# Kernel tuning notes

Hardware: AMD Instinct MI355X
Metric: run time of the kernel (lower is better)

The kernel has to match this reference:

```python
import jax, jax.numpy as jnp
import numpy as np

ALPHA = 0.2  # LeakyReLU negative slope
NEG_INF = -1e30


def _gat_layer(h, adj_mask, W, a, concat):
    # h: [N, Fin], W: [Fin, Fout], a: [2*Fout]
    Wh = h @ W                      # [N, Fout]
    F = W.shape[1]
    # e_ij = LeakyReLU(a[:F] . Wh_i + a[F:] . Wh_j)  -- equivalent to the
    # concat([Wh_i, Wh_j]) @ a formulation, without the N*N*2F tensor.
    src = Wh @ a[:F]                # [N]
    dst = Wh @ a[F:]                # [N]
    e = src[:, None] + dst[None, :]  # [N, N]
    e = jnp.where(e > 0, e, ALPHA * e)  # LeakyReLU
    e = jnp.where(adj_mask, e, NEG_INF)
    att = jax.nn.softmax(e, axis=1)  # [N, N]; dropout inactive (eval mode)
    h_prime = att @ Wh               # [N, Fout]
    return jax.nn.elu(h_prime) if concat else h_prime


def setup_inputs() -> dict:
    key = jax.random.key(0)
    ks = jax.random.split(key, 6)
    N, nfeat, nhid, nheads, nout = 4096, 512, 256, 4, 256
    x = jax.random.normal(ks[0], (N, nfeat), dtype=jnp.float32)
    adj = jax.random.randint(ks[1], (N, N), 0, 2, dtype=jnp.int32)
    W1 = jax.random.normal(ks[2], (nheads, nfeat, nhid), dtype=jnp.float32) * 0.05
    a1 = jax.random.normal(ks[3], (nheads, 2 * nhid), dtype=jnp.float32) * 0.05
    W2 = jax.random.normal(ks[4], (nhid * nheads, nout), dtype=jnp.float32) * 0.05
    a2 = jax.random.normal(ks[5], (2 * nout,), dtype=jnp.float32) * 0.05
    return {"x": x, "adj": adj, "W1": W1, "a1": a1, "W2": W2, "a2": a2}


def reference(x, adj, W1, a1, W2, a2):
    adj_mask = adj != 0  # [N, N] bool
    # Multi-head first layer (concat=True, ELU), vmapped over heads.
    heads = jax.vmap(lambda W, a: _gat_layer(x, adj_mask, W, a, True))(W1, a1)
    # heads: [nheads, N, nhid] -> concat along features: [N, nheads*nhid]
    h = jnp.transpose(heads, (1, 0, 2)).reshape(x.shape[0], -1)
    # Output attention layer (concat=False).
    return _gat_layer(h, adj_mask, W2, a2, False)
```

## Files before the change

kernel.cpp:

```cpp
#include <hip/hip_runtime.h>
#include <hip/hip_bf16.h>
#include <stdint.h>

#define ALPHA 0.2f
#define LOG2E 1.4426950408889634f

typedef __attribute__((ext_vector_type(4))) float f32x4;
typedef __attribute__((ext_vector_type(8))) __bf16 bf16x8;
typedef __attribute__((ext_vector_type(8))) unsigned short u16x8;
typedef __attribute__((ext_vector_type(4))) unsigned short u16x4;
typedef __attribute__((ext_vector_type(4))) unsigned int u32x4;

static __device__ __forceinline__ unsigned short f2bf(float f) {
  unsigned u = __builtin_bit_cast(unsigned, f);
  u += 0x7FFFu + ((u >> 16) & 1u);
  return (unsigned short)(u >> 16);
}
static __device__ __forceinline__ float bf2f(unsigned short h) {
  unsigned u = ((unsigned)h) << 16;
  return __builtin_bit_cast(float, u);
}
static __device__ __forceinline__ float exp2_hw(float x) {
  float r; asm("v_exp_f32 %0, %1" : "=v"(r) : "v"(x)); return r;
}
static __device__ __forceinline__ unsigned int cvt_pk_bf16(float lo, float hi) {
  unsigned int r; asm("v_cvt_pk_bf16_f32 %0, %1, %2" : "=v"(r) : "v"(lo), "v"(hi)); return r;
}
static __device__ __forceinline__ void gl_lds16(const void* g, void* lds) {
  __builtin_amdgcn_global_load_lds(
      (const __attribute__((address_space(1))) unsigned int*)g,
      (__attribute__((address_space(3))) unsigned int*)lds, 16, 0, 0);
}

#define PREP_PACK_END 16384
#define PREP_CAST_END 17408
#define PREP_T1_END   17920
#define PREP_T2_END   18176
#define PREP_WA1_END  18688
#define PREP_GRID     18944

__global__ void k_prep(const int* __restrict__ adj, unsigned int* __restrict__ bits,
                       const float* __restrict__ x, unsigned short* __restrict__ xb,
                       const float* __restrict__ W1, unsigned short* __restrict__ w1t,
                       const float* __restrict__ W2, unsigned short* __restrict__ w2t,
                       const float* __restrict__ a1, float* __restrict__ wa1,
                       const float* __restrict__ a2, float* __restrict__ wa2) {
  __shared__ float tsh[32][33];
  const int b = blockIdx.x, tid = threadIdx.x;
  if (b < PREP_PACK_END) {
    int row = b >> 2, qo = b & 3;
    const int4* ap = (const int4*)(adj + (size_t)row * 4096 + qo * 1024);
    int4 v = ap[tid];
    unsigned n = (unsigned)(v.x != 0) | ((unsigned)(v.y != 0) << 1) |
                 ((unsigned)(v.z != 0) << 2) | ((unsigned)(v.w != 0) << 3);
    unsigned char* nib = (unsigned char*)tsh;
    nib[tid] = (unsigned char)n;
    __syncthreads();
    if (tid < 32) {
      unsigned w = 0;
#pragma unroll
      for (int s = 0; s < 8; ++s) w |= ((unsigned)nib[tid * 8 + s]) << (4 * s);
      bits[(size_t)row * 128 + qo * 32 + tid] = w;
    }
  } else if (b < PREP_CAST_END) {
    int t = (b - PREP_PACK_END) * 256 + tid;
    const f32x4* p = (const f32x4*)(x + (long)t * 8);
    f32x4 va = p[0], vb = p[1];
    u16x8 o;
#pragma unroll
    for (int k = 0; k < 4; ++k) { o[k] = f2bf(va[k]); o[k + 4] = f2bf(vb[k]); }
    *(u16x8*)(xb + (long)t * 8) = o;
  } else if (b < PREP_T2_END) {
    const float* in; unsigned short* out; int K, N, bx, by, bz;
    if (b < PREP_T1_END) {
      int idx = b - PREP_CAST_END;
      bx = idx & 15; by = (idx >> 4) & 7; bz = idx >> 7;
      in = W1; out = w1t; K = 512; N = 256;
    } else {
      int idx = b - PREP_T1_END;
      bx = idx & 31; by = (idx >> 5) & 7; bz = 0;
      in = W2; out = w2t; K = 1024; N = 256;
    }
    long bs = (long)K * N;
    const float* inb = in + bz * bs;
    unsigned short* outb = out + bz * bs;
    int k0 = bx * 32, n0 = by * 32;
    int tx = tid & 31, ty = tid >> 5;
#pragma unroll
    for (int it = 0; it < 4; ++it)
      tsh[ty + it * 8][tx] = inb[(long)(k0 + ty + it * 8) * N + n0 + tx];
    __syncthreads();
#pragma unroll
    for (int it = 0; it < 4; ++it)
      outb[(long)(n0 + ty + it * 8) * K + k0 + tx] = f2bf(tsh[tx][ty + it * 8]);
  } else {
    const float* W; const float* a; float* wa; int headK;
    int bl;
    if (b < PREP_WA1_END) { bl = b - PREP_T2_END; W = W1; a = a1; wa = wa1; headK = 512; }
    else                  { bl = b - PREP_WA1_END; W = W2; a = a2; wa = wa2; headK = 1024; }
    const int F = 256;
    int w = (bl * 256 + tid) >> 6;
    int lane = tid & 63;
    int h = w / headK, fl = w % headK;
    const float* row = W + (size_t)w * F;
    const float* ah = a + (size_t)h * 2 * F;
    float s0 = 0.f, s1 = 0.f;
    for (int fo = lane; fo < F; fo += 64) {
      float wv = row[fo];
      s0 += wv * ah[fo];
      s1 += wv * ah[F + fo];
    }
#pragma unroll
    for (int off = 32; off; off >>= 1) {
      s0 += __shfl_xor(s0, off);
      s1 += __shfl_xor(s1, off);
    }
    if (lane == 0) {
      wa[(size_t)(h * 2 + 0) * headK + fl] = s0;
      wa[(size_t)(h * 2 + 1) * headK + fl] = s1;
    }
  }
}

static __device__ __forceinline__ void gemm_wh_body(
    const unsigned short* __restrict__ A, const unsigned short* __restrict__ BT,
    unsigned short* __restrict__ whT, int K, int i0, int fbase, char* lds) {
  unsigned short* As = (unsigned short*)lds;
  unsigned short* Bs = (unsigned short*)(lds + 8192);
  const int tid = threadIdx.x, lane = tid & 63, wid = tid >> 6;
  const int q = lane >> 4, l15 = lane & 15;
  const int wm = wid >> 1, wn = wid & 1;
  f32x4 acc[2][4] = {};
  const unsigned short* aRow = A + (long)(i0 + (tid >> 2)) * K + (tid & 3) * 8;
  const int cid1 = 256 + tid;
  const unsigned short* bRow0 = BT + (long)(fbase + (tid >> 2)) * K + (tid & 3) * 8;
  const unsigned short* bRow1 = BT + (long)(fbase + (cid1 >> 2)) * K + (cid1 & 3) * 8;

#define GSTAGE(PAR, KK)                                                        \
  gl_lds16(aRow + (KK), lds + (PAR) * 4096 + tid * 16);                        \
  gl_lds16(bRow0 + (KK), lds + 8192 + (PAR) * 8192 + tid * 16);                \
  gl_lds16(bRow1 + (KK), lds + 8192 + (PAR) * 8192 + cid1 * 16);

  GSTAGE(0, 0)
  asm volatile("s_waitcnt vmcnt(0)" ::: "memory");
  __builtin_amdgcn_sched_barrier(0);
  __builtin_amdgcn_s_barrier();
  for (int kk = 0; kk < K; kk += 32) {
    const int par = (kk >> 5) & 1;
    if (kk + 32 < K) { GSTAGE(par ^ 1, kk + 32) }
    bf16x8 af[2], bfr[4];
#pragma unroll
    for (int mi = 0; mi < 2; ++mi)
      af[mi] = *(const bf16x8*)&As[par * 2048 + (wm * 32 + mi * 16 + l15) * 32 + q * 8];
#pragma unroll
    for (int ni = 0; ni < 4; ++ni)
      bfr[ni] = *(const bf16x8*)&Bs[par * 4096 + (wn * 64 + ni * 16 + l15) * 32 + q * 8];
    __builtin_amdgcn_s_setprio(1);
#pragma unroll
    for (int mi = 0; mi < 2; ++mi)
#pragma unroll
      for (int ni = 0; ni < 4; ++ni)
        acc[mi][ni] = __builtin_amdgcn_mfma_f32_16x16x32_bf16(af[mi], bfr[ni], acc[mi][ni], 0, 0, 0);
    __builtin_amdgcn_s_setprio(0);
    asm volatile("s_waitcnt vmcnt(0)" ::: "memory");
    asm volatile("s_waitcnt lgkmcnt(0)" ::: "memory");
    __builtin_amdgcn_sched_barrier(0);
    __builtin_amdgcn_s_barrier();
    __builtin_amdgcn_sched_barrier(0);
  }
#undef GSTAGE
#pragma unroll
  for (int mi = 0; mi < 2; ++mi)
#pragma unroll
    for (int ni = 0; ni < 4; ++ni) {
      int ig = i0 + wm * 32 + mi * 16 + q * 4;
      int fg = fbase + wn * 64 + ni * 16 + l15;
      u16x4 v;
#pragma unroll
      for (int r = 0; r < 4; ++r) v[r] = f2bf(acc[mi][ni][r]);
      *(u16x4*)&whT[(long)fg * 4096 + ig] = v;
    }
}

__global__ void __launch_bounds__(256, 4)
k_l1(const unsigned short* __restrict__ xb, const unsigned short* __restrict__ w1t,
     unsigned short* __restrict__ whT1, const float* __restrict__ wa,
     float* __restrict__ srcv, float* __restrict__ dstv, float* __restrict__ dstva) {
  __shared__ char lds[24576];
  const int b = blockIdx.x, tid = threadIdx.x;
  if (b < 512) {
    int i0 = (b & 63) * 64;
    int fbase = (b >> 7) * 256 + ((b >> 6) & 1) * 128;
    gemm_wh_body(xb, w1t, whT1, 512, i0, fbase, lds);
    return;
  }
  const int mb = b - 512;
  int lane = tid & 63, wid = tid >> 6;
  float wv[8][8];
#pragma unroll
  for (int v = 0; v < 8; ++v)
#pragma unroll
    for (int j = 0; j < 8; ++j) wv[v][j] = wa[v * 512 + lane * 8 + j];
  int base = (mb * 4 + wid) * 4;
  for (int rr = 0; rr < 4; ++rr) {
    int i = base + rr;
    u16x8 xv = *(const u16x8*)(xb + (size_t)i * 512 + lane * 8);
    float xf[8];
#pragma unroll
    for (int j = 0; j < 8; ++j) xf[j] = bf2f(xv[j]);
    float s[8] = {};
#pragma unroll
    for (int v = 0; v < 8; ++v)
#pragma unroll
      for (int j = 0; j < 8; ++j) s[v] += xf[j] * wv[v][j];
#pragma unroll
    for (int v = 0; v < 8; ++v)
#pragma unroll
      for (int off = 32; off; off >>= 1) s[v] += __shfl_xor(s[v], off);
    if (lane == 0) {
#pragma unroll
      for (int h = 0; h < 4; ++h) {
        srcv[h * 4096 + i] = s[h * 2] * LOG2E;
        float d = s[h * 2 + 1] * LOG2E;
        dstv[h * 4096 + i] = d;
        dstva[h * 4096 + i] = ALPHA * d;
      }
    }
  }
}

__global__ void __launch_bounds__(256, 4)
k_l2(const unsigned short* __restrict__ h1, const unsigned short* __restrict__ w2t,
     unsigned short* __restrict__ whT2, const float* __restrict__ wa,
     float* __restrict__ srcv, float* __restrict__ dstv, float* __restrict__ dstva) {
  __shared__ char lds[24576];
  const int b = blockIdx.x;
  if (b < 128) {
    int i0 = (b & 63) * 64;
    int fbase = ((b >> 6) & 1) * 128;
    gemm_wh_body(h1, w2t, whT2, 1024, i0, fbase, lds);
    return;
  }
  const int mb = b - 128;
  int lane = threadIdx.x & 63, wid = threadIdx.x >> 6;
  float wv[2][16];
#pragma unroll
  for (int v = 0; v < 2; ++v)
#pragma unroll
    for (int j = 0; j < 16; ++j) wv[v][j] = wa[v * 1024 + lane * 16 + j];
  int base = (mb * 4 + wid) * 4;
  for (int rr = 0; rr < 4; ++rr) {
    int i = base + rr;
    u16x8 x0 = *(const u16x8*)(h1 + (size_t)i * 1024 + lane * 16);
    u16x8 x1 = *(const u16x8*)(h1 + (size_t)i * 1024 + lane * 16 + 8);
    float s0 = 0.f, s1 = 0.f;
#pragma unroll
    for (int j = 0; j < 8; ++j) {
      float a0 = bf2f(x0[j]), a1 = bf2f(x1[j]);
      s0 += a0 * wv[0][j] + a1 * wv[0][j + 8];
      s1 += a0 * wv[1][j] + a1 * wv[1][j + 8];
    }
#pragma unroll
    for (int off = 32; off; off >>= 1) {
      s0 += __shfl_xor(s0, off);
      s1 += __shfl_xor(s1, off);
    }
    if (lane == 0) {
      srcv[i] = s0 * LOG2E;
      float d = s1 * LOG2E;
      dstv[i] = d;
      dstva[i] = ALPHA * d;
    }
  }
}


#define STAGE(PAR)                                                             \
  _Pragma("unroll")                                                            \
  for (int it = 0; it < 8; ++it)                                               \
    gl_lds16(wh_head + sidx + it * 131072u,                                    \
             (char*)&Bs[PAR][0] + (it * 256 + tid) * 16);                      \
  sidx += 64;

#define PREFETCH(DZ, DA, WB)                                                   \
  _Pragma("unroll")                                                            \
  for (int c4 = 0; c4 < 4; ++c4) {                                             \
    DZ[c4] = *(const f32x4*)(dzp + c4 * 4);                                    \
    DA[c4] = *(const f32x4*)(dap + c4 * 4);                                    \
  }                                                                            \
  WB = *browp;                                                                 \
  dzp += 64; dap += 64; browp += 2;

#define PCOMP(WB, DZ, DA)                                                      \
  {                                                                            \
    unsigned wbv = (WB >> shift) & 0xFFFFu;                                    \
    _Pragma("unroll")                                                          \
    for (int c8 = 0; c8 < 2; ++c8) {                                           \
      float pe[8];                                                             \
      _Pragma("unroll")                                                        \
      for (int jj = 0; jj < 8; ++jj) {                                         \
        float e = fmaxf(sm + DZ[c8 * 2 + (jj >> 2)][jj & 3],                   \
                        am + DA[c8 * 2 + (jj >> 2)][jj & 3]);                  \
        e = (wbv & (1u << (c8 * 8 + jj))) ? e : -1e30f;                        \
        pe[jj] = exp2_hw(e);                                                   \
      }                                                                        \
      u32x4 pv;                                                                \
      pv[0] = cvt_pk_bf16(pe[0], pe[1]);                                       \
      pv[1] = cvt_pk_bf16(pe[2], pe[3]);                                       \
      pv[2] = cvt_pk_bf16(pe[4], pe[5]);                                       \
      pv[3] = cvt_pk_bf16(pe[6], pe[7]);                                       \
      lsum += ((pe[0] + pe[1]) + (pe[2] + pe[3])) +                            \
              ((pe[4] + pe[5]) + (pe[6] + pe[7]));                             \
      if (c8) pvB = pv; else pvA = pv;                                         \
    }                                                                          \
  }

#define PSTO(PAR)                                                              \
  *(u32x4*)&Ps[PAR][prow * 64 + ((2 * kq + 0) ^ (prow & 7)) * 8] = pvA;        \
  *(u32x4*)&Ps[PAR][prow * 64 + ((2 * kq + 1) ^ (prow & 7)) * 8] = pvB;

#define DOMFMA(PAR)                                                            \
  {                                                                            \
    _Pragma("unroll")                                                          \
    for (int s = 0; s < 2; ++s) {                                              \
      bf16x8 af[4], bfr[4];                                                    \
      _Pragma("unroll")                                                        \
      for (int mi = 0; mi < 4; ++mi)                                           \
        af[mi] = *(const bf16x8*)&Ps[PAR][(mi * 16 + l15) * 64 +               \
                                          ((s * 4 + q) ^ (l15 & 7)) * 8];      \
      _Pragma("unroll")                                                        \
      for (int ni = 0; ni < 4; ++ni) {                                         \
        int f = wid * 64 + ni * 16 + l15;                                      \
        int slot = (s * 4 + q) ^ (l15 & 7);                                    \
        bfr[ni] = *(const bf16x8*)&Bs[PAR][f * 64 + slot * 8];                 \
      }                                                                        \
      __builtin_amdgcn_s_setprio(1);                                           \
      _Pragma("unroll")                                                        \
      for (int mi = 0; mi < 4; ++mi)                                           \
        _Pragma("unroll")                                                      \
        for (int ni = 0; ni < 4; ++ni)                                         \
          acc[mi][ni] = __builtin_amdgcn_mfma_f32_16x16x32_bf16(               \
              af[mi], bfr[ni], acc[mi][ni], 0, 0, 0);                          \
      __builtin_amdgcn_s_setprio(0);                                           \
    }                                                                          \
  }

#define STEP_SYNC                                                              \
  asm volatile("s_waitcnt vmcnt(9)" ::: "memory");                             \
  asm volatile("s_waitcnt lgkmcnt(0)" ::: "memory");                           \
  __builtin_amdgcn_sched_barrier(0);                                           \
  __builtin_amdgcn_s_barrier();                                                \
  __builtin_amdgcn_sched_barrier(0);

#define BODY(PAR, DZC, DAC, WBC, DZN, DAN, WBN)                                \
  {                                                                            \
    STAGE(PAR ^ 1)                                                             \
    __builtin_amdgcn_sched_barrier(0);     \
    PREFETCH(DZN, DAN, WBN)                                                    \
    PCOMP(WBC, DZC, DAC)                                                       \
    DOMFMA(PAR)                                                                \
    PSTO(PAR ^ 1)                                                              \
    STEP_SYNC                                                                  \
  }

template <int JS, int H, int OC>
__global__ void __launch_bounds__(256, 2)
k_attn4(const unsigned short* __restrict__ whT, const unsigned int* __restrict__ bits,
        const float* __restrict__ srcv, const float* __restrict__ dstv,
        const float* __restrict__ dstva,
        float* __restrict__ Opart, float* __restrict__ Lpart) {
  static_assert(H * JS == 8, "group size must be 8");
  __shared__ unsigned short Bs[2][256 * 64];
  __shared__ unsigned short Ps[2][64 * 64];
  const int tid = threadIdx.x, lane = tid & 63, wid = tid >> 6;
  const int q = lane >> 4, l15 = lane & 15;
  const int bid = blockIdx.x;
  const int g = bid & 7;
  const int head = g & (H - 1);
  const int js = g / H;
  const int i0 = (bid >> 3) * 64;
  const int jbase = js * (4096 / JS);
  constexpr int JSTEPS = (4096 / JS) / 64;

  const unsigned short* wh_head = whT + (size_t)head * 256 * 4096;
  const int prow = tid & 63, kq = tid >> 6;

  float dmax;
  {
    float* dred = (float*)&Ps[0][0];
    const float* dp = dstv + head * 4096;
    float lm = -1e30f;
#pragma unroll
    for (int k = 0; k < 4; ++k) {
      f32x4 v = *(const f32x4*)(dp + (tid + k * 256) * 4);
      lm = fmaxf(fmaxf(lm, fmaxf(v[0], v[1])), fmaxf(v[2], v[3]));
    }
#pragma unroll
    for (int off = 32; off; off >>= 1) lm = fmaxf(lm, __shfl_xor(lm, off));
    if (lane == 0) dred[wid] = lm;
    __syncthreads();
    dmax = fmaxf(fmaxf(dred[0], dred[1]), fmaxf(dred[2], dred[3]));
    __syncthreads();
  }

  float src_r = srcv[head * 4096 + i0 + prow];
  float m_r;
  { float xm = src_r + dmax; m_r = fmaxf(xm, ALPHA * xm); }
  const float sm = src_r - m_r;
  const float am = ALPHA * src_r - m_r;
  float lsum = 0.f;
  f32x4 acc[4][4] = {};

  const int srow = tid >> 3;
  unsigned sidx = (unsigned)(srow * 4096 + jbase + ((tid & 7) ^ (srow & 7)) * 8);
  const float* dzp = dstv + head * 4096 + jbase + kq * 16;
  const float* dap = dstva + head * 4096 + jbase + kq * 16;
  const unsigned int* browp = bits + (size_t)(i0 + prow) * 128 + (jbase >> 5) + (kq >> 1);
  const int shift = (kq & 1) * 16;

  f32x4 dzA[4], daA[4], dzB[4], daB[4];
  unsigned wbA, wbB;
  u32x4 pvA, pvB;

  PREFETCH(dzA, daA, wbA)
  __builtin_amdgcn_sched_barrier(0);
  STAGE(0)
  __builtin_amdgcn_sched_barrier(0);
  PREFETCH(dzB, daB, wbB)
  PCOMP(wbA, dzA, daA)
  PSTO(0)
  STEP_SYNC

  for (int t = 0; t < JSTEPS - 3; t += 2) {
    BODY(0, dzB, daB, wbB, dzA, daA, wbA)
    BODY(1, dzA, daA, wbA, dzB, daB, wbB)
  }
  BODY(0, dzB, daB, wbB, dzA, daA, wbA)
  DOMFMA(1)

  __syncthreads();
  float* Lred = (float*)&Ps[0][0];
  Lred[kq * 64 + prow] = lsum;
  __syncthreads();
  if (tid < 64)
    Lpart[(size_t)(js * H + head) * 4096 + i0 + tid] =
        Lred[tid] + Lred[64 + tid] + Lred[128 + tid] + Lred[192 + tid];
  float* Ob = Opart + (size_t)js * 4096 * OC + head * 256;
#pragma unroll
  for (int mi = 0; mi < 4; ++mi)
#pragma unroll
    for (int ni = 0; ni < 4; ++ni) {
      int i = i0 + mi * 16 + q * 4;
      int col = wid * 64 + ni * 16 + l15;
#pragma unroll
      for (int r = 0; r < 4; ++r)
        Ob[(size_t)(i + r) * OC + col] = acc[mi][ni][r];
    }
}

__global__ void __launch_bounds__(256) k_comb1(const float* __restrict__ Op,
                                               const float* __restrict__ Lp,
                                               unsigned short* __restrict__ h1) {
  int gidx = blockIdx.x * 256 + threadIdx.x;
  int i = gidx >> 8, c0 = (gidx & 255) * 4;
  int h = c0 >> 8;
  float l = Lp[h * 4096 + i] + Lp[(4 + h) * 4096 + i];
  float inv = 1.f / l;
  f32x4 p0 = *(const f32x4*)(Op + (size_t)i * 1024 + c0);
  f32x4 p1 = *(const f32x4*)(Op + (size_t)4096 * 1024 + (size_t)i * 1024 + c0);
  u16x4 o;
#pragma unroll
  for (int r = 0; r < 4; ++r) {
    float v = (p0[r] + p1[r]) * inv;
    v = v > 0.f ? v : (__expf(v) - 1.f);
    o[r] = f2bf(v);
  }
  *(u16x4*)(h1 + (size_t)i * 1024 + c0) = o;
}

__global__ void __launch_bounds__(256) k_comb2(const float* __restrict__ Op,
                                               const float* __restrict__ Lp,
                                               float* __restrict__ out) {
  int gidx = blockIdx.x * 256 + threadIdx.x;
  int i = gidx >> 6, c0 = (gidx & 63) * 4;
  float l = 0.f;
#pragma unroll
  for (int js = 0; js < 8; ++js) l += Lp[js * 4096 + i];
  f32x4 s = {0.f, 0.f, 0.f, 0.f};
#pragma unroll
  for (int js = 0; js < 8; ++js)
    s += *(const f32x4*)(Op + (size_t)js * 4096 * 256 + (size_t)i * 256 + c0);
  float inv = 1.f / l;
  f32x4 o;
#pragma unroll
  for (int r = 0; r < 4; ++r) o[r] = s[r] * inv;
  *(f32x4*)(out + (size_t)i * 256 + c0) = o;
}

extern "C" void kernel_launch(void* const* d_in, const int* in_sizes, int n_in,
                              void* d_out, int out_size, void* d_ws, size_t ws_size,
                              hipStream_t stream) {
  const float* x  = (const float*)d_in[0];
  const int* adj  = (const int*)d_in[1];
  const float* W1 = (const float*)d_in[2];
  const float* a1 = (const float*)d_in[3];
  const float* W2 = (const float*)d_in[4];
  const float* a2 = (const float*)d_in[5];

  char* ws = (char*)d_ws;
  size_t off = 0;
  auto alloc = [&](size_t bytes) {
    void* p = ws + off;
    off = (off + bytes + 255) & ~(size_t)255;
    return p;
  };
  unsigned int*   bits = (unsigned int*)  alloc((size_t)4096 * 128 * 4);
  unsigned short* xb   = (unsigned short*)alloc((size_t)4096 * 512 * 2);
  unsigned short* w1t  = (unsigned short*)alloc((size_t)4 * 256 * 512 * 2);
  unsigned short* w2t  = (unsigned short*)alloc((size_t)256 * 1024 * 2);
  unsigned short* whT1 = (unsigned short*)alloc((size_t)1024 * 4096 * 2);
  unsigned short* h1   = (unsigned short*)alloc((size_t)4096 * 1024 * 2);
  unsigned short* whT2 = (unsigned short*)alloc((size_t)256 * 4096 * 2);
  float* wa1  = (float*)alloc((size_t)8 * 512 * 4);
  float* wa2  = (float*)alloc((size_t)2 * 1024 * 4);
  float* src1 = (float*)alloc(4 * 4096 * 4);
  float* dst1 = (float*)alloc(4 * 4096 * 4);
  float* dst1a = (float*)alloc(4 * 4096 * 4);
  float* src2 = (float*)alloc(4096 * 4);
  float* dst2 = (float*)alloc(4096 * 4);
  float* dst2a = (float*)alloc(4096 * 4);
  float* Lp1  = (float*)alloc((size_t)8 * 4096 * 4);
  float* Lp2  = (float*)alloc((size_t)8 * 4096 * 4);
  float* Opart = (float*)alloc((size_t)2 * 4096 * 1024 * 4);

  k_prep<<<dim3(PREP_GRID), dim3(256), 0, stream>>>(
      adj, bits, x, xb, W1, w1t, W2, w2t, a1, wa1, a2, wa2);

  k_l1<<<dim3(768), dim3(256), 0, stream>>>(xb, w1t, whT1, wa1, src1, dst1, dst1a);
  k_attn4<2, 4, 1024><<<dim3(512), dim3(256), 0, stream>>>(whT1, bits, src1, dst1, dst1a, Opart, Lp1);
  k_comb1<<<dim3(4096), dim3(256), 0, stream>>>(Opart, Lp1, h1);

  k_l2<<<dim3(384), dim3(256), 0, stream>>>(h1, w2t, whT2, wa2, src2, dst2, dst2a);
  k_attn4<8, 1, 256><<<dim3(512), dim3(256), 0, stream>>>(whT2, bits, src2, dst2, dst2a, Opart, Lp2);
  k_comb2<<<dim3(1024), dim3(256), 0, stream>>>(Opart, Lp2, (float*)d_out);
}
```

Baseline: 226.7 us.

## Double attention block to 512 threads with 2x4 wave tiling

Launches the attention kernel with 8 waves instead of 4. Each wave now computes a 32x64 output tile instead of 64x64, and each thread builds 8 probabilities per step instead of 16. Staging loads, prefetch and the wait counts are adjusted to match. The aim is more waves in flight to hide exp and load latency, at the cost of more barrier participants and less MFMA work per wave per LDS fragment load.

```diff
diff --git a/kernel.cpp b/kernel.cpp
--- a/kernel.cpp
+++ b/kernel.cpp
@@ -277,66 +277,58 @@
 
 #define STAGE(PAR)                                                             \
   _Pragma("unroll")                                                            \
-  for (int it = 0; it < 8; ++it)                                               \
-    gl_lds16(wh_head + sidx + it * 131072u,                                    \
-             (char*)&Bs[PAR][0] + (it * 256 + tid) * 16);                      \
+  for (int it = 0; it < 4; ++it)                                               \
+    gl_lds16(wh_head + sidx + it * 262144u,                                    \
+             (char*)&Bs[PAR][0] + (it * 512 + tid) * 16);                      \
   sidx += 64;
 
 #define PREFETCH(DZ, DA, WB)                                                   \
-  _Pragma("unroll")                                                            \
-  for (int c4 = 0; c4 < 4; ++c4) {                                             \
-    DZ[c4] = *(const f32x4*)(dzp + c4 * 4);                                    \
-    DA[c4] = *(const f32x4*)(dap + c4 * 4);                                    \
-  }                                                                            \
+  DZ[0] = *(const f32x4*)(dzp);                                                \
+  DZ[1] = *(const f32x4*)(dzp + 4);                                            \
+  DA[0] = *(const f32x4*)(dap);                                                \
+  DA[1] = *(const f32x4*)(dap + 4);                                            \
   WB = *browp;                                                                 \
   dzp += 64; dap += 64; browp += 2;
 
 #define PCOMP(WB, DZ, DA)                                                      \
   {                                                                            \
-    unsigned wbv = (WB >> shift) & 0xFFFFu;                                    \
+    unsigned wbv = (WB >> shift) & 0xFFu;                                      \
+    float pe[8];                                                               \
     _Pragma("unroll")                                                          \
-    for (int c8 = 0; c8 < 2; ++c8) {                                           \
-      float pe[8];                                                             \
-      _Pragma("unroll")                                                        \
-      for (int jj = 0; jj < 8; ++jj) {                                         \
-        float e = fmaxf(sm + DZ[c8 * 2 + (jj >> 2)][jj & 3],                   \
-                        am + DA[c8 * 2 + (jj >> 2)][jj & 3]);                  \
-        e = (wbv & (1u << (c8 * 8 + jj))) ? e : -1e30f;                        \
-        pe[jj] = exp2_hw(e);                                                   \
-      }                                                                        \
-      u32x4 pv;                                                                \
-      pv[0] = cvt_pk_bf16(pe[0], pe[1]);                                       \
-      pv[1] = cvt_pk_bf16(pe[2], pe[3]);                                       \
-      pv[2] = cvt_pk_bf16(pe[4], pe[5]);                                       \
-      pv[3] = cvt_pk_bf16(pe[6], pe[7]);                                       \
-      lsum += ((pe[0] + pe[1]) + (pe[2] + pe[3])) +                            \
-              ((pe[4] + pe[5]) + (pe[6] + pe[7]));                             \
-      if (c8) pvB = pv; else pvA = pv;                                         \
+    for (int jj = 0; jj < 8; ++jj) {                                           \
+      float e = fmaxf(sm + DZ[jj >> 2][jj & 3], am + DA[jj >> 2][jj & 3]);     \
+      e = (wbv & (1u << jj)) ? e : -1e30f;                  \
+      pe[jj] = exp2_hw(e);                                                     \
     }                                                                          \
+    pvA[0] = cvt_pk_bf16(pe[0], pe[1]);                                        \
+    pvA[1] = cvt_pk_bf16(pe[2], pe[3]);                                        \
+    pvA[2] = cvt_pk_bf16(pe[4], pe[5]);                                        \
+    pvA[3] = cvt_pk_bf16(pe[6], pe[7]);                                        \
+    lsum += ((pe[0] + pe[1]) + (pe[2] + pe[3])) +                              \
+            ((pe[4] + pe[5]) + (pe[6] + pe[7]));                               \
   }
 
 #define PSTO(PAR)                                                              \
-  *(u32x4*)&Ps[PAR][prow * 64 + ((2 * kq + 0) ^ (prow & 7)) * 8] = pvA;        \
-  *(u32x4*)&Ps[PAR][prow * 64 + ((2 * kq + 1) ^ (prow & 7)) * 8] = pvB;
+  *(u32x4*)&Ps[PAR][prow * 64 + (kq ^ (prow & 7)) * 8] = pvA;
 
 #define DOMFMA(PAR)                                                            \
   {                                                                            \
     _Pragma("unroll")                                                          \
     for (int s = 0; s < 2; ++s) {                                              \
-      bf16x8 af[4], bfr[4];                                                    \
+      bf16x8 af[2], bfr[4];                                                    \
       _Pragma("unroll")                                                        \
-      for (int mi = 0; mi < 4; ++mi)                                           \
-        af[mi] = *(const bf16x8*)&Ps[PAR][(mi * 16 + l15) * 64 +               \
+      for (int mi = 0; mi < 2; ++mi)                                           \
+        af[mi] = *(const bf16x8*)&Ps[PAR][(wm * 32 + mi * 16 + l15) * 64 +     \
                                           ((s * 4 + q) ^ (l15 & 7)) * 8];      \
       _Pragma("unroll")                                                        \
       for (int ni = 0; ni < 4; ++ni) {                                         \
-        int f = wid * 64 + ni * 16 + l15;                                      \
+        int f = wn * 64 + ni * 16 + l15;                                       \
         int slot = (s * 4 + q) ^ (l15 & 7);                                    \
         bfr[ni] = *(const bf16x8*)&Bs[PAR][f * 64 + slot * 8];                 \
       }                                                                        \
       __builtin_amdgcn_s_setprio(1);                                           \
       _Pragma("unroll")                                                        \
-      for (int mi = 0; mi < 4; ++mi)                                           \
+      for (int mi = 0; mi < 2; ++mi)                                           \
         _Pragma("unroll")                                                      \
         for (int ni = 0; ni < 4; ++ni)                                         \
           acc[mi][ni] = __builtin_amdgcn_mfma_f32_16x16x32_bf16(               \
@@ -346,7 +338,7 @@
   }
 
 #define STEP_SYNC                                                              \
-  asm volatile("s_waitcnt vmcnt(9)" ::: "memory");                             \
+  asm volatile("s_waitcnt vmcnt(5)" ::: "memory");                             \
   asm volatile("s_waitcnt lgkmcnt(0)" ::: "memory");                           \
   __builtin_amdgcn_sched_barrier(0);                                           \
   __builtin_amdgcn_s_barrier();                                                \
@@ -364,8 +356,8 @@
   }
 
 template <int JS, int H, int OC>
-__global__ void __launch_bounds__(256, 2)
-k_attn4(const unsigned short* __restrict__ whT, const unsigned int* __restrict__ bits,
+__global__ void __launch_bounds__(512, 4)
+k_attn8(const unsigned short* __restrict__ whT, const unsigned int* __restrict__ bits,
         const float* __restrict__ srcv, const float* __restrict__ dstv,
         const float* __restrict__ dstva,
         float* __restrict__ Opart, float* __restrict__ Lpart) {
@@ -374,6 +366,7 @@
   __shared__ unsigned short Ps[2][64 * 64];
   const int tid = threadIdx.x, lane = tid & 63, wid = tid >> 6;
   const int q = lane >> 4, l15 = lane & 15;
+  const int wm = wid & 1, wn = wid >> 1;
   const int bid = blockIdx.x;
   const int g = bid & 7;
   const int head = g & (H - 1);
@@ -389,17 +382,17 @@
   {
     float* dred = (float*)&Ps[0][0];
     const float* dp = dstv + head * 4096;
-    float lm = -1e30f;
-#pragma unroll
-    for (int k = 0; k < 4; ++k) {
-      f32x4 v = *(const f32x4*)(dp + (tid + k * 256) * 4);
-      lm = fmaxf(fmaxf(lm, fmaxf(v[0], v[1])), fmaxf(v[2], v[3]));
-    }
+    f32x4 v0 = *(const f32x4*)(dp + tid * 8);
+    f32x4 v1 = *(const f32x4*)(dp + tid * 8 + 4);
+    float lm = fmaxf(fmaxf(fmaxf(v0[0], v0[1]), fmaxf(v0[2], v0[3])),
+                     fmaxf(fmaxf(v1[0], v1[1]), fmaxf(v1[2], v1[3])));
 #pragma unroll
     for (int off = 32; off; off >>= 1) lm = fmaxf(lm, __shfl_xor(lm, off));
     if (lane == 0) dred[wid] = lm;
     __syncthreads();
-    dmax = fmaxf(fmaxf(dred[0], dred[1]), fmaxf(dred[2], dred[3]));
+    float m01 = fmaxf(dred[0], dred[1]), m23 = fmaxf(dred[2], dred[3]);
+    float m45 = fmaxf(dred[4], dred[5]), m67 = fmaxf(dred[6], dred[7]);
+    dmax = fmaxf(fmaxf(m01, m23), fmaxf(m45, m67));
     __syncthreads();
   }
 
@@ -409,18 +402,18 @@
   const float sm = src_r - m_r;
   const float am = ALPHA * src_r - m_r;
   float lsum = 0.f;
-  f32x4 acc[4][4] = {};
+  f32x4 acc[2][4] = {};
 
   const int srow = tid >> 3;
   unsigned sidx = (unsigned)(srow * 4096 + jbase + ((tid & 7) ^ (srow & 7)) * 8);
-  const float* dzp = dstv + head * 4096 + jbase + kq * 16;
-  const float* dap = dstva + head * 4096 + jbase + kq * 16;
-  const unsigned int* browp = bits + (size_t)(i0 + prow) * 128 + (jbase >> 5) + (kq >> 1);
-  const int shift = (kq & 1) * 16;
-
-  f32x4 dzA[4], daA[4], dzB[4], daB[4];
+  const float* dzp = dstv + head * 4096 + jbase + kq * 8;
+  const float* dap = dstva + head * 4096 + jbase + kq * 8;
+  const unsigned int* browp = bits + (size_t)(i0 + prow) * 128 + (jbase >> 5) + (kq >> 2);
+  const int shift = (kq & 3) * 8;
+
+  f32x4 dzA[2], daA[2], dzB[2], daB[2];
   unsigned wbA, wbB;
-  u32x4 pvA, pvB;
+  u32x4 pvA;
 
   PREFETCH(dzA, daA, wbA)
   __builtin_amdgcn_sched_barrier(0);
@@ -442,16 +435,19 @@
   float* Lred = (float*)&Ps[0][0];
   Lred[kq * 64 + prow] = lsum;
   __syncthreads();
-  if (tid < 64)
-    Lpart[(size_t)(js * H + head) * 4096 + i0 + tid] =
-        Lred[tid] + Lred[64 + tid] + Lred[128 + tid] + Lred[192 + tid];
+  if (tid < 64) {
+    float s = 0.f;
+#pragma unroll
+    for (int k = 0; k < 8; ++k) s += Lred[k * 64 + tid];
+    Lpart[(size_t)(js * H + head) * 4096 + i0 + tid] = s;
+  }
   float* Ob = Opart + (size_t)js * 4096 * OC + head * 256;
 #pragma unroll
-  for (int mi = 0; mi < 4; ++mi)
+  for (int mi = 0; mi < 2; ++mi)
 #pragma unroll
     for (int ni = 0; ni < 4; ++ni) {
-      int i = i0 + mi * 16 + q * 4;
-      int col = wid * 64 + ni * 16 + l15;
+      int i = i0 + wm * 32 + mi * 16 + q * 4;
+      int col = wn * 64 + ni * 16 + l15;
 #pragma unroll
       for (int r = 0; r < 4; ++r)
         Ob[(size_t)(i + r) * OC + col] = acc[mi][ni][r];
@@ -537,10 +533,10 @@
       adj, bits, x, xb, W1, w1t, W2, w2t, a1, wa1, a2, wa2);
 
   k_l1<<<dim3(768), dim3(256), 0, stream>>>(xb, w1t, whT1, wa1, src1, dst1, dst1a);
-  k_attn4<2, 4, 1024><<<dim3(512), dim3(256), 0, stream>>>(whT1, bits, src1, dst1, dst1a, Opart, Lp1);
+  k_attn8<2, 4, 1024><<<dim3(512), dim3(512), 0, stream>>>(whT1, bits, src1, dst1, dst1a, Opart, Lp1);
   k_comb1<<<dim3(4096), dim3(256), 0, stream>>>(Opart, Lp1, h1);
 
   k_l2<<<dim3(384), dim3(256), 0, stream>>>(h1, w2t, whT2, wa2, src2, dst2, dst2a);
-  k_attn4<8, 1, 256><<<dim3(512), dim3(256), 0, stream>>>(whT2, bits, src2, dst2, dst2a, Opart, Lp2);
+  k_attn8<8, 1, 256><<<dim3(512), dim3(512), 0, stream>>>(whT2, bits, src2, dst2, dst2a, Opart, Lp2);
   k_comb2<<<dim3(1024), dim3(256), 0, stream>>>(Opart, Lp2, (float*)d_out);
 }
```

New measurement: 234.3 us. +3.3%, slower.
